# Performance work log

Hardware: AMD Instinct MI355X
Metric: run time of the kernel (lower is better)

Reference implementation:

```python
import jax, jax.numpy as jnp
import numpy as np

LRU_DIM = 256
HIDDEN = 256
H = 64
N = LRU_DIM // H  # 4 (even, per assert)
R_MIN, R_MAX, MAX_PHASE = 0.9, 0.999, 6.28
BSZ, T = 8, 4096


def _rotate_half(x):
    # interleaved pairs: [x0,x1,x2,x3,...] -> [-x1,x0,-x3,x2,...]
    r = jnp.stack([-x[..., 1::2], x[..., 0::2]], axis=-1)
    return r.reshape(x.shape)


def _mix_sequence(gamma, thetas, Us):
    # gamma: scalar, thetas: (N/2,), Us: (T,B,N) -> (T,B,N)
    Tlen = Us.shape[0]
    gammas = jnp.broadcast_to(gamma, (Tlen,))
    ths = jnp.broadcast_to(thetas, (Tlen,) + thetas.shape)

    def binf(a, b):
        gi, ti, xi = a
        gj, tj, xj = b
        theta = jnp.repeat(tj, 2, axis=-1)            # (T, N): [t0,t0,t1,t1,...]
        sin = jnp.sin(theta)[..., None, :]            # (T,1,N)
        cos = jnp.cos(theta)[..., None, :]
        acc = gj[..., None, None] * (cos * xi + sin * _rotate_half(xi)) + xj
        return (gi * gj, ti + tj, acc)

    _, _, res = jax.lax.associative_scan(binf, (gammas, ths, Us), axis=0)
    return res


def setup_inputs() -> dict:
    key = jax.random.key(0)
    ks = jax.random.split(key, 7)
    scale = 1.0 / np.sqrt(HIDDEN + LRU_DIM)
    u = jax.random.normal(ks[0], (BSZ, HIDDEN, T), dtype=jnp.float32)
    thetas_log = jnp.log(jax.random.uniform(ks[1], (H, N // 2), minval=0.01, maxval=1.0) * MAX_PHASE).astype(jnp.float32)
    P_param = (jax.random.normal(ks[2], (H, N, N), dtype=jnp.float32) / np.sqrt(LRU_DIM + N)).astype(jnp.float32)
    B_param = (jax.random.normal(ks[3], (H, N, HIDDEN), dtype=jnp.float32) * scale).astype(jnp.float32)
    C = (jax.random.normal(ks[4], (HIDDEN, LRU_DIM), dtype=jnp.float32) * scale).astype(jnp.float32)
    D = jax.random.normal(ks[5], (HIDDEN,), dtype=jnp.float32)
    u1 = jax.random.uniform(ks[6], (H,))
    gamma_log = (np.log(-np.log(R_MAX)) + u1 * (np.log(-np.log(R_MIN)) - np.log(-np.log(R_MAX)))).astype(jnp.float32)
    return {"u": u, "thetas_log": thetas_log, "P_param": P_param,
            "B_param": B_param, "C": C, "D": D, "gamma_log": gamma_log}


def reference(u, thetas_log, P_param, B_param, C, D, gamma_log):
    Bsz, hidden, Tlen = u.shape
    ut = jnp.transpose(u, (0, 2, 1))                       # (B,T,Dh)
    gamma = jnp.exp(-jnp.exp(gamma_log))                   # (H,)
    trace_per_head = jnp.sum(B_param * B_param, axis=(1, 2))  # tr(B B^T) per head
    norm = jnp.sqrt((1.0 - gamma ** 2) / trace_per_head)
    B_norm = norm[:, None, None] * B_param                 # (H,N,Dh)
    skew = P_param - jnp.swapaxes(P_param, 1, 2)
    P = jax.vmap(jax.scipy.linalg.expm)(skew)              # (H,N,N), orthogonal
    Us = jnp.einsum('HnD,BTD->HTBn', B_norm, ut)           # (H,T,B,N)
    Us = jnp.einsum('HNn,HTBn->HTBN', P, Us)               # == einsum with P^T as in torch
    thetas = jnp.exp(thetas_log)                           # (H,N/2)
    y = jax.vmap(_mix_sequence)(gamma, thetas, Us)         # (H,T,B,N)
    y = jnp.einsum('HNn,HTBN->HTBn', P, y)
    y = jnp.transpose(y, (2, 1, 0, 3)).reshape(Bsz, Tlen, -1)  # (B,T,lru_dim)
    y = jnp.einsum('Dn,BTn->BTD', C, y) + D * ut
    return jnp.transpose(y, (0, 2, 1))                     # (B,Dh,T)
```

## Files before the change

kernel.cpp:

```cpp
#include <hip/hip_runtime.h>
#include <hip/hip_bf16.h>
#include <math.h>


typedef __attribute__((ext_vector_type(8))) short short8;
typedef __attribute__((ext_vector_type(4))) float f32x4;

#define TLEN 4096
#define LCH 32
#define NCH 128
#define BSZ 8
#define LDK 264
#define LDW 132

constexpr int MB_OFF   = 0;
constexpr int CB_OFF   = 32768;
constexpr int A1_OFF   = 65536;
constexpr int AL_OFF   = 65792;
constexpr int TOT_OFF  = 66048;
constexpr int CAR_OFF  = TOT_OFF + NCH * BSZ * 256;
constexpr int PL_OFF   = CAR_OFF + NCH * BSZ * 256;
constexpr int NORM_OFF = PL_OFF + 1024;

__device__ __forceinline__ float bfbits2f(unsigned int bits16) {
  union { unsigned int u; float f; } v; v.u = bits16 << 16; return v.f;
}
__device__ __forceinline__ unsigned int f2bfbits(float f) {
  union { float f; unsigned int u; } v; v.f = f;
  return (v.u + 0x7fffu + ((v.u >> 16) & 1u)) >> 16;
}
__device__ __forceinline__ unsigned int pack2(float x, float y) {
  return f2bfbits(x) | (f2bfbits(y) << 16);
}

__global__ __launch_bounds__(256) void k0a_precompute(
    const float* __restrict__ thetas_log, const float* __restrict__ P_param,
    const float* __restrict__ B_param, const float* __restrict__ gamma_log,
    float* __restrict__ ws) {
  __shared__ float tracep[64][4];
  __shared__ double gamma_d[64];
  const int tid = threadIdx.x;
  {
    int h = tid >> 2, q = tid & 3;
    const float* bp = B_param + (h * 4 + q) * 256;
    float s = 0.f;
    for (int i = 0; i < 256; ++i) { float v = bp[i]; s += v * v; }
    tracep[h][q] = s;
  }
  __syncthreads();
  if (tid < 64) {
    int h = tid;
    double g = exp(-exp((double)gamma_log[h]));
    gamma_d[h] = g;
    double tr = (double)tracep[h][0] + tracep[h][1] + tracep[h][2] + tracep[h][3];
    ws[NORM_OFF + h] = (float)sqrt((1.0 - g * g) / tr);
    double A[4][4], E[4][4], Tm[4][4];
    for (int i = 0; i < 4; ++i)
      for (int j = 0; j < 4; ++j)
        A[i][j] = (double)P_param[h * 16 + i * 4 + j] - (double)P_param[h * 16 + j * 4 + i];
    double fro = 0.0;
    for (int i = 0; i < 4; ++i) for (int j = 0; j < 4; ++j) fro += A[i][j] * A[i][j];
    fro = sqrt(fro);
    int s = 0;
    while (fro > 0.25 && s < 30) { fro *= 0.5; ++s; }
    double scl = 1.0;
    for (int q2 = 0; q2 < s; ++q2) scl *= 0.5;
    for (int i = 0; i < 4; ++i) for (int j = 0; j < 4; ++j) A[i][j] *= scl;
    for (int i = 0; i < 4; ++i)
      for (int j = 0; j < 4; ++j) { E[i][j] = (i == j) ? 1.0 : 0.0; Tm[i][j] = E[i][j]; }
    for (int k = 1; k <= 16; ++k) {
      double Tn[4][4];
      for (int i = 0; i < 4; ++i)
        for (int j = 0; j < 4; ++j) {
          double acc = 0.0;
          for (int m = 0; m < 4; ++m) acc += Tm[i][m] * A[m][j];
          Tn[i][j] = acc / (double)k;
        }
      for (int i = 0; i < 4; ++i)
        for (int j = 0; j < 4; ++j) { Tm[i][j] = Tn[i][j]; E[i][j] += Tn[i][j]; }
    }
    for (int q2 = 0; q2 < s; ++q2) {
      double E2[4][4];
      for (int i = 0; i < 4; ++i)
        for (int j = 0; j < 4; ++j) {
          double acc = 0.0;
          for (int m = 0; m < 4; ++m) acc += E[i][m] * E[m][j];
          E2[i][j] = acc;
        }
      for (int i = 0; i < 4; ++i) for (int j = 0; j < 4; ++j) E[i][j] = E2[i][j];
    }
    for (int i = 0; i < 4; ++i)
      for (int j = 0; j < 4; ++j) ws[PL_OFF + h * 16 + i * 4 + j] = (float)E[i][j];
  }
  __syncthreads();
  if (tid < 128) {
    int h = tid >> 1, p = tid & 1;
    double th = exp((double)thetas_log[h * 2 + p]);
    double g = gamma_d[h];
    double ar = g * cos(th), ai = g * sin(th);
    ((float2*)(ws + A1_OFF))[tid] = make_float2((float)ar, (float)ai);
    double xr = ar, xi = ai;
    for (int q = 0; q < 5; ++q) {
      double nr = xr * xr - xi * xi, ni = 2.0 * xr * xi;
      xr = nr; xi = ni;
    }
    ((float2*)(ws + AL_OFF))[tid] = make_float2((float)xr, (float)xi);
  }
}

__global__ __launch_bounds__(256) void k0b_mats(
    const float* __restrict__ B_param, const float* __restrict__ C,
    float* __restrict__ ws) {
  const float* Pl  = ws + PL_OFF;
  const float* nrm = ws + NORM_OFF;
  unsigned short* Mbf = (unsigned short*)(ws + MB_OFF);
  unsigned short* Cbf = (unsigned short*)(ws + CB_OFF);
  const int blk = blockIdx.x, tid = threadIdx.x;
  if (blk < 16) {
    for (int rr = 0; rr < 16; ++rr) {
      int r = blk * 16 + rr, h = r >> 2, N = r & 3;
      float acc = 0.f;
      for (int n = 0; n < 4; ++n)
        acc += Pl[h * 16 + N * 4 + n] * B_param[(h * 4 + n) * 256 + tid];
      Mbf[r * 256 + tid] = (unsigned short)f2bfbits(nrm[h] * acc);
    }
  } else {
    int h = tid >> 2, N = tid & 3;
    for (int rr = 0; rr < 16; ++rr) {
      int Do = (blk - 16) * 16 + rr;
      float acc = 0.f;
      for (int n = 0; n < 4; ++n)
        acc += C[Do * 256 + (tid & ~3) + n] * Pl[h * 16 + N * 4 + n];
      Cbf[Do * 256 + tid] = (unsigned short)f2bfbits(acc);
    }
  }
}

__global__ __launch_bounds__(256) void k1_tot(
    const float* __restrict__ u, float* __restrict__ ws) {
  __shared__ __align__(16) unsigned char smem[LCH * LDK * 2];
  unsigned short* us = (unsigned short*)smem;
  unsigned int*   wd = (unsigned int*)smem;

  const int c = blockIdx.x, b = blockIdx.y;
  const int t0 = c * LCH;
  const int tid = threadIdx.x;
  const int L = tid & 63;
  const int w = __builtin_amdgcn_readfirstlane(tid >> 6);
  const int qh = L >> 4, l15 = L & 15;

  {
    const int kbase = tid >> 3, t4 = (tid & 7) * 4;
#pragma unroll
    for (int i = 0; i < 8; ++i) {
      int d = kbase + i * 32;
      float4 v = *(const float4*)(u + (size_t)(b * 256 + d) * TLEN + t0 + t4);
      float vv[4] = {v.x, v.y, v.z, v.w};
#pragma unroll
      for (int dt = 0; dt < 4; ++dt)
        us[(t4 + dt) * LDK + (d ^ (dt << 3))] = (unsigned short)f2bfbits(vv[dt]);
    }
  }
  __syncthreads();

  f32x4 acc[4][2];
#pragma unroll
  for (int rt = 0; rt < 4; ++rt)
#pragma unroll
    for (int tt = 0; tt < 2; ++tt) acc[rt][tt] = (f32x4){0.f, 0.f, 0.f, 0.f};
  {
    const unsigned short* Mbf = (const unsigned short*)(ws + MB_OFF);
#pragma unroll
    for (int ks = 0; ks < 8; ++ks) {
      short8 af[4], bf[2];
#pragma unroll
      for (int rt = 0; rt < 4; ++rt)
        af[rt] = *(const short8*)(Mbf + (size_t)(w * 64 + rt * 16 + l15) * 256 + ks * 32 + qh * 8);
#pragma unroll
      for (int tt = 0; tt < 2; ++tt) {
        int row = tt * 16 + l15;
        int col = (ks * 32 + qh * 8) ^ ((row & 3) << 3);
        bf[tt] = *(const short8*)(us + row * LDK + col);
      }
#pragma unroll
      for (int rt = 0; rt < 4; ++rt)
#pragma unroll
        for (int tt = 0; tt < 2; ++tt)
          acc[rt][tt] = __builtin_amdgcn_mfma_f32_16x16x32_bf16(af[rt], bf[tt], acc[rt][tt], 0, 0, 0);
    }
  }
  __syncthreads();

#pragma unroll
  for (int rt = 0; rt < 4; ++rt) {
    int pbase = w * 32 + rt * 8 + qh * 2;
#pragma unroll
    for (int tt = 0; tt < 2; ++tt) {
      int t = tt * 16 + l15;
      f32x4 a4 = acc[rt][tt];
      *(uint2*)&wd[t * LDW + pbase] = make_uint2(pack2(a4[0], a4[1]), pack2(a4[2], a4[3]));
    }
  }
  __syncthreads();

  if (tid < 128) {
    const int p = tid;
    float2 a = ((const float2*)(ws + A1_OFF))[p];
    float zr = 0.f, zi = 0.f;
#pragma unroll
    for (int t = 0; t < LCH; ++t) {
      unsigned int wv = wd[t * LDW + p];
      float wr = bfbits2f(wv & 0xffffu), wi = bfbits2f(wv >> 16);
      float nr = fmaf(a.x, zr, fmaf(-a.y, zi, wr));
      float ni = fmaf(a.x, zi, fmaf(a.y, zr, wi));
      zr = nr; zi = ni;
    }
    ((float2*)(ws + TOT_OFF))[(c * BSZ + b) * 128 + p] = make_float2(zr, zi);
  }
}

__global__ __launch_bounds__(128) void k2_carry(float* __restrict__ ws) {
  const int b = blockIdx.x, p = threadIdx.x;
  const float2 aL = ((const float2*)(ws + AL_OFF))[p];
  const float2* Tot = (const float2*)(ws + TOT_OFF);
  float2* Car = (float2*)(ws + CAR_OFF);
  float cr = 0.f, ci = 0.f;
  Car[(0 * BSZ + b) * 128 + p] = make_float2(0.f, 0.f);
  for (int c = 1; c < NCH; ++c) {
    float2 tv = Tot[((c - 1) * BSZ + b) * 128 + p];
    float nr = fmaf(aL.x, cr, fmaf(-aL.y, ci, tv.x));
    float ni = fmaf(aL.x, ci, fmaf(aL.y, cr, tv.y));
    cr = nr; ci = ni;
    Car[(c * BSZ + b) * 128 + p] = make_float2(cr, ci);
  }
}

__global__ __launch_bounds__(256) void k3_fused(
    const float* __restrict__ u, const float* __restrict__ Dv,
    const float* __restrict__ ws, float* __restrict__ out) {
  __shared__ __align__(16) unsigned char smem[2 * LCH * LDK * 2];
  unsigned short* us = (unsigned short*)smem;
  unsigned int*   wd = (unsigned int*)(smem + LCH * LDK * 2);

  const int c = blockIdx.x, b = blockIdx.y;
  const int t0 = c * LCH;
  const int tid = threadIdx.x;
  const int L = tid & 63;
  const int w = __builtin_amdgcn_readfirstlane(tid >> 6);
  const int qh = L >> 4, l15 = L & 15;

  {
    const int kbase = tid >> 3, t4 = (tid & 7) * 4;
#pragma unroll
    for (int i = 0; i < 8; ++i) {
      int d = kbase + i * 32;
      float4 v = *(const float4*)(u + (size_t)(b * 256 + d) * TLEN + t0 + t4);
      float vv[4] = {v.x, v.y, v.z, v.w};
#pragma unroll
      for (int dt = 0; dt < 4; ++dt)
        us[(t4 + dt) * LDK + (d ^ (dt << 3))] = (unsigned short)f2bfbits(vv[dt]);
    }
  }
  __syncthreads();

  f32x4 acc[4][2];
#pragma unroll
  for (int rt = 0; rt < 4; ++rt)
#pragma unroll
    for (int tt = 0; tt < 2; ++tt) acc[rt][tt] = (f32x4){0.f, 0.f, 0.f, 0.f};
  {
    const unsigned short* Mbf = (const unsigned short*)(ws + MB_OFF);
#pragma unroll
    for (int ks = 0; ks < 8; ++ks) {
      short8 af[4], bf[2];
#pragma unroll
      for (int rt = 0; rt < 4; ++rt)
        af[rt] = *(const short8*)(Mbf + (size_t)(w * 64 + rt * 16 + l15) * 256 + ks * 32 + qh * 8);
#pragma unroll
      for (int tt = 0; tt < 2; ++tt) {
        int row = tt * 16 + l15;
        int col = (ks * 32 + qh * 8) ^ ((row & 3) << 3);
        bf[tt] = *(const short8*)(us + row * LDK + col);
      }
#pragma unroll
      for (int rt = 0; rt < 4; ++rt)
#pragma unroll
        for (int tt = 0; tt < 2; ++tt)
          acc[rt][tt] = __builtin_amdgcn_mfma_f32_16x16x32_bf16(af[rt], bf[tt], acc[rt][tt], 0, 0, 0);
    }
  }

#pragma unroll
  for (int rt = 0; rt < 4; ++rt) {
    int pbase = w * 32 + rt * 8 + qh * 2;
#pragma unroll
    for (int tt = 0; tt < 2; ++tt) {
      int t = tt * 16 + l15;
      f32x4 a4 = acc[rt][tt];
      *(uint2*)&wd[t * LDW + pbase] = make_uint2(pack2(a4[0], a4[1]), pack2(a4[2], a4[3]));
    }
  }
  __syncthreads();

  if (tid < 128) {
    const int p = tid;
    float2 a = ((const float2*)(ws + A1_OFF))[p];
    float2 cv = ((const float2*)(ws + CAR_OFF))[(c * BSZ + b) * 128 + p];
    float zr = cv.x, zi = cv.y;
#pragma unroll
    for (int t = 0; t < LCH; ++t) {
      unsigned int wv = wd[t * LDW + p];
      float wr = bfbits2f(wv & 0xffffu), wi = bfbits2f(wv >> 16);
      float nr = fmaf(a.x, zr, fmaf(-a.y, zi, wr));
      float ni = fmaf(a.x, zi, fmaf(a.y, zr, wi));
      zr = nr; zi = ni;
      wd[t * LDW + p] = pack2(zr, zi);
    }
  }
  __syncthreads();

#pragma unroll
  for (int rt = 0; rt < 4; ++rt)
#pragma unroll
    for (int tt = 0; tt < 2; ++tt) acc[rt][tt] = (f32x4){0.f, 0.f, 0.f, 0.f};
  {
    const unsigned short* Cbf = (const unsigned short*)(ws + CB_OFF);
    const unsigned short* zs  = (const unsigned short*)wd;
#pragma unroll
    for (int ks = 0; ks < 8; ++ks) {
      short8 af[4], bf[2];
#pragma unroll
      for (int rt = 0; rt < 4; ++rt)
        af[rt] = *(const short8*)(Cbf + (size_t)(w * 64 + rt * 16 + l15) * 256 + ks * 32 + qh * 8);
#pragma unroll
      for (int tt = 0; tt < 2; ++tt)
        bf[tt] = *(const short8*)(zs + (tt * 16 + l15) * LDK + ks * 32 + qh * 8);
#pragma unroll
      for (int rt = 0; rt < 4; ++rt)
#pragma unroll
        for (int tt = 0; tt < 2; ++tt)
          acc[rt][tt] = __builtin_amdgcn_mfma_f32_16x16x32_bf16(af[rt], bf[tt], acc[rt][tt], 0, 0, 0);
    }
  }

#pragma unroll
  for (int rt = 0; rt < 4; ++rt) {
    int Dbase = w * 64 + rt * 16 + qh * 4;
    float dv[4];
#pragma unroll
    for (int q = 0; q < 4; ++q) dv[q] = Dv[Dbase + q];
#pragma unroll
    for (int tt = 0; tt < 2; ++tt) {
      int t = tt * 16 + l15;
      f32x4 a4 = acc[rt][tt];
      size_t obase = (size_t)(b * 256 + Dbase) * TLEN + t0 + t;
#pragma unroll
      for (int q = 0; q < 4; ++q) {
        float uu = bfbits2f(us[t * LDK + ((Dbase + q) ^ ((t & 3) << 3))]);
        out[obase + (size_t)q * TLEN] = a4[q] + dv[q] * uu;
      }
    }
  }
}

extern "C" void kernel_launch(void* const* d_in, const int* in_sizes, int n_in,
                              void* d_out, int out_size, void* d_ws, size_t ws_size,
                              hipStream_t stream) {
  const float* u          = (const float*)d_in[0];
  const float* thetas_log = (const float*)d_in[1];
  const float* P_param    = (const float*)d_in[2];
  const float* B_param    = (const float*)d_in[3];
  const float* C          = (const float*)d_in[4];
  const float* Dvec       = (const float*)d_in[5];
  const float* gamma_log  = (const float*)d_in[6];
  float* out = (float*)d_out;
  float* ws  = (float*)d_ws;

  hipLaunchKernelGGL(k0a_precompute, dim3(1), dim3(256), 0, stream,
                     thetas_log, P_param, B_param, gamma_log, ws);
  hipLaunchKernelGGL(k0b_mats, dim3(32), dim3(256), 0, stream, B_param, C, ws);
  hipLaunchKernelGGL(k1_tot, dim3(NCH, BSZ), dim3(256), 0, stream, u, ws);
  hipLaunchKernelGGL(k2_carry, dim3(BSZ), dim3(128), 0, stream, ws);
  hipLaunchKernelGGL(k3_fused, dim3(NCH, BSZ), dim3(256), 0, stream, u, Dvec, ws, out);
}
```

Measured before the change: 188.9 us.

## Fuse chunk-total, carry and output kernels into one decoupled-lookback scan kernel

Merges the three-kernel chunked scan (chunk totals, serial carry, recompute-and-output) into a single kernel. Each block publishes its chunk total with a release flag, waits on all predecessor flags, and computes its carry directly as a sum of precomputed powers of the decay applied to earlier totals. It then corrects the local scan with precomputed per-step powers. This removes the recompute of the input projection GEMM, two kernel launches and the serial carry kernel. In exchange it relies on all earlier blocks being resident or finished (a spin-wait deadlock risk if scheduling is not in order), adds an O(c) carry sum per block, and changes the rounding of the carry.

Result: slower. 250.7 us (+32.7%).

```diff
diff --git a/kernel.cpp b/kernel.cpp
--- a/kernel.cpp
+++ b/kernel.cpp
@@ -16,10 +16,11 @@
 constexpr int MB_OFF   = 0;
 constexpr int CB_OFF   = 32768;
 constexpr int A1_OFF   = 65536;
-constexpr int AL_OFF   = 65792;
-constexpr int TOT_OFF  = 66048;
-constexpr int CAR_OFF  = TOT_OFF + NCH * BSZ * 256;
-constexpr int PL_OFF   = CAR_OFF + NCH * BSZ * 256;
+constexpr int AP_OFF   = 65792;
+constexpr int ALP_OFF  = AP_OFF + 32 * 256;
+constexpr int TOT_OFF  = ALP_OFF + 128 * 256;
+constexpr int FLG_OFF  = TOT_OFF + NCH * BSZ * 256;
+constexpr int PL_OFF   = FLG_OFF + BSZ * NCH;
 constexpr int NORM_OFF = PL_OFF + 1024;
 
 __device__ __forceinline__ float bfbits2f(unsigned int bits16) {
@@ -41,11 +42,18 @@
   __shared__ double gamma_d[64];
   const int tid = threadIdx.x;
   {
-    int h = tid >> 2, q = tid & 3;
-    const float* bp = B_param + (h * 4 + q) * 256;
+    int* fl = (int*)(ws + FLG_OFF);
+    fl[tid] = 0; fl[tid + 256] = 0; fl[tid + 512] = 0; fl[tid + 768] = 0;
+  }
+  {
+    const float4* bp = (const float4*)(B_param + tid * 256);
     float s = 0.f;
-    for (int i = 0; i < 256; ++i) { float v = bp[i]; s += v * v; }
-    tracep[h][q] = s;
+#pragma unroll 8
+    for (int i = 0; i < 64; ++i) {
+      float4 v = bp[i];
+      s += v.x * v.x + v.y * v.y + v.z * v.z + v.w * v.w;
+    }
+    tracep[tid >> 2][tid & 3] = s;
   }
   __syncthreads();
   if (tid < 64) {
@@ -99,12 +107,23 @@
     double g = gamma_d[h];
     double ar = g * cos(th), ai = g * sin(th);
     ((float2*)(ws + A1_OFF))[tid] = make_float2((float)ar, (float)ai);
+    float2* Apw = (float2*)(ws + AP_OFF);
     double xr = ar, xi = ai;
-    for (int q = 0; q < 5; ++q) {
-      double nr = xr * xr - xi * xi, ni = 2.0 * xr * xi;
+    Apw[tid] = make_float2((float)xr, (float)xi);
+    for (int j = 2; j <= 32; ++j) {
+      double nr = xr * ar - xi * ai, ni = xr * ai + xi * ar;
       xr = nr; xi = ni;
-    }
-    ((float2*)(ws + AL_OFF))[tid] = make_float2((float)xr, (float)xi);
+      Apw[(j - 1) * 128 + tid] = make_float2((float)xr, (float)xi);
+    }
+    double br = xr, bi = xi;
+    float2* ALp = (float2*)(ws + ALP_OFF);
+    xr = 1.0; xi = 0.0;
+    ALp[tid] = make_float2(1.f, 0.f);
+    for (int k = 1; k < NCH; ++k) {
+      double nr = xr * br - xi * bi, ni = xr * bi + xi * br;
+      xr = nr; xi = ni;
+      ALp[k * 128 + tid] = make_float2((float)xr, (float)xi);
+    }
   }
 }
 
@@ -136,11 +155,12 @@
   }
 }
 
-__global__ __launch_bounds__(256) void k1_tot(
-    const float* __restrict__ u, float* __restrict__ ws) {
-  __shared__ __align__(16) unsigned char smem[LCH * LDK * 2];
+__global__ __launch_bounds__(256, 4) void main_rotssm(
+    const float* __restrict__ u, const float* __restrict__ Dv,
+    float* __restrict__ ws, float* __restrict__ out) {
+  __shared__ __align__(16) unsigned char smem[2 * LCH * LDK * 2];
   unsigned short* us = (unsigned short*)smem;
-  unsigned int*   wd = (unsigned int*)smem;
+  unsigned int*   wd = (unsigned int*)(smem + LCH * LDK * 2);
 
   const int c = blockIdx.x, b = blockIdx.y;
   const int t0 = c * LCH;
@@ -189,7 +209,6 @@
           acc[rt][tt] = __builtin_amdgcn_mfma_f32_16x16x32_bf16(af[rt], bf[tt], acc[rt][tt], 0, 0, 0);
     }
   }
-  __syncthreads();
 
 #pragma unroll
   for (int rt = 0; rt < 4; ++rt) {
@@ -207,106 +226,6 @@
     const int p = tid;
     float2 a = ((const float2*)(ws + A1_OFF))[p];
     float zr = 0.f, zi = 0.f;
-#pragma unroll
-    for (int t = 0; t < LCH; ++t) {
-      unsigned int wv = wd[t * LDW + p];
-      float wr = bfbits2f(wv & 0xffffu), wi = bfbits2f(wv >> 16);
-      float nr = fmaf(a.x, zr, fmaf(-a.y, zi, wr));
-      float ni = fmaf(a.x, zi, fmaf(a.y, zr, wi));
-      zr = nr; zi = ni;
-    }
-    ((float2*)(ws + TOT_OFF))[(c * BSZ + b) * 128 + p] = make_float2(zr, zi);
-  }
-}
-
-__global__ __launch_bounds__(128) void k2_carry(float* __restrict__ ws) {
-  const int b = blockIdx.x, p = threadIdx.x;
-  const float2 aL = ((const float2*)(ws + AL_OFF))[p];
-  const float2* Tot = (const float2*)(ws + TOT_OFF);
-  float2* Car = (float2*)(ws + CAR_OFF);
-  float cr = 0.f, ci = 0.f;
-  Car[(0 * BSZ + b) * 128 + p] = make_float2(0.f, 0.f);
-  for (int c = 1; c < NCH; ++c) {
-    float2 tv = Tot[((c - 1) * BSZ + b) * 128 + p];
-    float nr = fmaf(aL.x, cr, fmaf(-aL.y, ci, tv.x));
-    float ni = fmaf(aL.x, ci, fmaf(aL.y, cr, tv.y));
-    cr = nr; ci = ni;
-    Car[(c * BSZ + b) * 128 + p] = make_float2(cr, ci);
-  }
-}
-
-__global__ __launch_bounds__(256) void k3_fused(
-    const float* __restrict__ u, const float* __restrict__ Dv,
-    const float* __restrict__ ws, float* __restrict__ out) {
-  __shared__ __align__(16) unsigned char smem[2 * LCH * LDK * 2];
-  unsigned short* us = (unsigned short*)smem;
-  unsigned int*   wd = (unsigned int*)(smem + LCH * LDK * 2);
-
-  const int c = blockIdx.x, b = blockIdx.y;
-  const int t0 = c * LCH;
-  const int tid = threadIdx.x;
-  const int L = tid & 63;
-  const int w = __builtin_amdgcn_readfirstlane(tid >> 6);
-  const int qh = L >> 4, l15 = L & 15;
-
-  {
-    const int kbase = tid >> 3, t4 = (tid & 7) * 4;
-#pragma unroll
-    for (int i = 0; i < 8; ++i) {
-      int d = kbase + i * 32;
-      float4 v = *(const float4*)(u + (size_t)(b * 256 + d) * TLEN + t0 + t4);
-      float vv[4] = {v.x, v.y, v.z, v.w};
-#pragma unroll
-      for (int dt = 0; dt < 4; ++dt)
-        us[(t4 + dt) * LDK + (d ^ (dt << 3))] = (unsigned short)f2bfbits(vv[dt]);
-    }
-  }
-  __syncthreads();
-
-  f32x4 acc[4][2];
-#pragma unroll
-  for (int rt = 0; rt < 4; ++rt)
-#pragma unroll
-    for (int tt = 0; tt < 2; ++tt) acc[rt][tt] = (f32x4){0.f, 0.f, 0.f, 0.f};
-  {
-    const unsigned short* Mbf = (const unsigned short*)(ws + MB_OFF);
-#pragma unroll
-    for (int ks = 0; ks < 8; ++ks) {
-      short8 af[4], bf[2];
-#pragma unroll
-      for (int rt = 0; rt < 4; ++rt)
-        af[rt] = *(const short8*)(Mbf + (size_t)(w * 64 + rt * 16 + l15) * 256 + ks * 32 + qh * 8);
-#pragma unroll
-      for (int tt = 0; tt < 2; ++tt) {
-        int row = tt * 16 + l15;
-        int col = (ks * 32 + qh * 8) ^ ((row & 3) << 3);
-        bf[tt] = *(const short8*)(us + row * LDK + col);
-      }
-#pragma unroll
-      for (int rt = 0; rt < 4; ++rt)
-#pragma unroll
-        for (int tt = 0; tt < 2; ++tt)
-          acc[rt][tt] = __builtin_amdgcn_mfma_f32_16x16x32_bf16(af[rt], bf[tt], acc[rt][tt], 0, 0, 0);
-    }
-  }
-
-#pragma unroll
-  for (int rt = 0; rt < 4; ++rt) {
-    int pbase = w * 32 + rt * 8 + qh * 2;
-#pragma unroll
-    for (int tt = 0; tt < 2; ++tt) {
-      int t = tt * 16 + l15;
-      f32x4 a4 = acc[rt][tt];
-      *(uint2*)&wd[t * LDW + pbase] = make_uint2(pack2(a4[0], a4[1]), pack2(a4[2], a4[3]));
-    }
-  }
-  __syncthreads();
-
-  if (tid < 128) {
-    const int p = tid;
-    float2 a = ((const float2*)(ws + A1_OFF))[p];
-    float2 cv = ((const float2*)(ws + CAR_OFF))[(c * BSZ + b) * 128 + p];
-    float zr = cv.x, zi = cv.y;
 #pragma unroll
     for (int t = 0; t < LCH; ++t) {
       unsigned int wv = wd[t * LDW + p];
@@ -315,6 +234,42 @@
       float ni = fmaf(a.x, zi, fmaf(a.y, zr, wi));
       zr = nr; zi = ni;
       wd[t * LDW + p] = pack2(zr, zi);
+    }
+    ((float2*)(ws + TOT_OFF))[(c * BSZ + b) * 128 + p] = make_float2(zr, zi);
+    __threadfence();
+  }
+  __syncthreads();
+  if (tid == 0)
+    __hip_atomic_store((int*)(ws + FLG_OFF) + b * NCH + c, 1,
+                       __ATOMIC_RELEASE, __HIP_MEMORY_SCOPE_AGENT);
+
+  if (c > 0) {
+    if (tid < c) {
+      const int* fl = (const int*)(ws + FLG_OFF) + b * NCH + tid;
+      while (__hip_atomic_load(fl, __ATOMIC_ACQUIRE, __HIP_MEMORY_SCOPE_AGENT) == 0)
+        __builtin_amdgcn_s_sleep(1);
+    }
+    __syncthreads();
+    if (tid < 128) {
+      const int p = tid;
+      const float2* ALp = (const float2*)(ws + ALP_OFF);
+      const float2* Tot = (const float2*)(ws + TOT_OFF);
+      float cr = 0.f, ci = 0.f;
+      for (int cp = 0; cp < c; ++cp) {
+        float2 al = ALp[(c - 1 - cp) * 128 + p];
+        float2 tv = Tot[(cp * BSZ + b) * 128 + p];
+        cr = fmaf(al.x, tv.x, fmaf(-al.y, tv.y, cr));
+        ci = fmaf(al.x, tv.y, fmaf(al.y, tv.x, ci));
+      }
+      const float2* Apw = (const float2*)(ws + AP_OFF);
+#pragma unroll
+      for (int t = 0; t < LCH; ++t) {
+        float2 ap = Apw[t * 128 + p];
+        unsigned int wv = wd[t * LDW + p];
+        float sr = fmaf(ap.x, cr, fmaf(-ap.y, ci, bfbits2f(wv & 0xffffu)));
+        float si = fmaf(ap.x, ci, fmaf(ap.y, cr, bfbits2f(wv >> 16)));
+        wd[t * LDW + p] = pack2(sr, si);
+      }
     }
   }
   __syncthreads();
@@ -379,7 +334,6 @@
   hipLaunchKernelGGL(k0a_precompute, dim3(1), dim3(256), 0, stream,
                      thetas_log, P_param, B_param, gamma_log, ws);
   hipLaunchKernelGGL(k0b_mats, dim3(32), dim3(256), 0, stream, B_param, C, ws);
-  hipLaunchKernelGGL(k1_tot, dim3(NCH, BSZ), dim3(256), 0, stream, u, ws);
-  hipLaunchKernelGGL(k2_carry, dim3(BSZ), dim3(128), 0, stream, ws);
-  hipLaunchKernelGGL(k3_fused, dim3(NCH, BSZ), dim3(256), 0, stream, u, Dvec, ws, out);
-}
+  hipLaunchKernelGGL(main_rotssm, dim3(NCH, BSZ), dim3(256), 0, stream,
+                     u, Dvec, ws, out);
+}
```
